# Performance work log

Measured on AMD Instinct MI355X. Metric: run time of the kernel, lower is better.

The kernel has to match this reference:

```python
import jax, jax.numpy as jnp
import numpy as np

B, Q, K, D = 16, 2048, 2048, 512


def setup_inputs() -> dict:
    key = jax.random.key(0)
    kq, kk, kv, kl = jax.random.split(key, 4)
    queries = jax.random.normal(kq, (B, Q, D), dtype=jnp.float32)
    keys = jax.random.normal(kk, (B, K, D), dtype=jnp.float32)
    values = jax.random.normal(kv, (B, K, D), dtype=jnp.float32)
    # lengths in [1, K] so no row is fully masked
    valid_lens = jax.random.randint(kl, (B,), 1, K + 1, dtype=jnp.int32)
    return {"queries": queries, "keys": keys, "values": values, "valid_lens": valid_lens}


def reference(queries, keys, values, valid_lens):
    # scores: [B, Q, K]
    scale = 1.0 / jnp.sqrt(jnp.asarray(queries.shape[-1], queries.dtype))
    scores = jnp.einsum('bqd,bkd->bqk', queries, keys) * scale
    # 1D valid_lens: per-batch key-length mask (positions >= len are masked)
    key_pos = jnp.arange(scores.shape[-1])  # [K]
    mask = key_pos[None, None, :] >= valid_lens[:, None, None]  # [B, 1->Q, K]
    scores = jnp.where(mask, -jnp.inf, scores)
    weights = jax.nn.softmax(scores, axis=-1)  # [B, Q, K]
    # dropout is identity in eval mode (deterministic reference)
    context = jnp.einsum('bqk,bkd->bqd', weights, values)  # [B, Q, D]
    return context, weights
```

## Files before the change

kernel.cpp:

```cpp
#include <hip/hip_runtime.h>
#include <stdint.h>

typedef __bf16 bf16_t;
typedef bf16_t bf16x8 __attribute__((ext_vector_type(8)));
typedef float f32x4 __attribute__((ext_vector_type(4)));

#define NB 16
#define NQ 2048
#define NK 2048
#define ND 512
#define SCALE 0.04419417382415922f

typedef __attribute__((address_space(3))) uint32_t lds_u32;
typedef __attribute__((address_space(1))) const uint32_t glb_u32;

__device__ __forceinline__ float4 ld4(const float* p) { return *(const float4*)p; }

__device__ __forceinline__ f32x4 mfma16(bf16x8 a, bf16x8 b, f32x4 c) {
  return __builtin_amdgcn_mfma_f32_16x16x32_bf16(a, b, c, 0, 0, 0);
}

__global__ __launch_bounds__(256) void qkprep_kernel(const float* __restrict__ Qf,
                                                     const float* __restrict__ Kf,
                                                     bf16_t* __restrict__ Qb,
                                                     bf16_t* __restrict__ Kb) {
  int x = blockIdx.x;
  int b = blockIdx.y;
  const float* src = blockIdx.z ? Kf : Qf;
  bf16_t* dst = blockIdx.z ? Kb : Qb;
  int rt = x >> 4, kt = x & 15;
  const float* s = src + ((size_t)b * 2048 + (size_t)rt * 128) * 512 + kt * 32;
  bf16_t* dtile = dst + (((size_t)b * 16 + rt) * 16 + kt) * 4096;
  int t = threadIdx.x;
#pragma unroll
  for (int i = 0; i < 2; ++i) {
    int d = i * 256 + t;
    int r = d >> 2, slot = d & 3;
    int c = slot ^ ((r >> 1) & 3);
    const float* p = s + (size_t)r * 512 + c * 8;
    float4 v0 = ld4(p), v1 = ld4(p + 4);
    bf16x8 o;
    o[0] = (bf16_t)v0.x; o[1] = (bf16_t)v0.y; o[2] = (bf16_t)v0.z; o[3] = (bf16_t)v0.w;
    o[4] = (bf16_t)v1.x; o[5] = (bf16_t)v1.y; o[6] = (bf16_t)v1.z; o[7] = (bf16_t)v1.w;
    *(bf16x8*)(dtile + (size_t)d * 8) = o;
  }
}

__global__ __launch_bounds__(256) void vt_kernel(const float* __restrict__ V,
                                                 bf16_t* __restrict__ VT,
                                                 const int* __restrict__ lens) {
  int kb = blockIdx.x, b = blockIdx.y;
  if (kb * 32 >= lens[b]) return;
  const float* vsrc = V + ((size_t)b * NK + kb * 32) * ND;
  bf16_t* dst = VT + ((size_t)(b * 64 + kb)) * (512 * 32);
  __shared__ alignas(16) bf16_t Ls[32][128];
  int t = threadIdx.x;
  for (int dbase = 0; dbase < ND; dbase += 128) {
#pragma unroll
    for (int i = 0; i < 4; ++i) {
      int p = i * 256 + t;
      int k = p >> 5, c4 = p & 31;
      float4 v = ld4(vsrc + (size_t)k * ND + dbase + c4 * 4);
      union { bf16_t h[4]; uint2 u; } pk;
      pk.h[0] = (bf16_t)v.x; pk.h[1] = (bf16_t)v.y;
      pk.h[2] = (bf16_t)v.z; pk.h[3] = (bf16_t)v.w;
      *(uint2*)(&Ls[k][c4 * 4]) = pk.u;
    }
    __syncthreads();
    int d = dbase + (t >> 1);
    int h = t & 1;
    int sr = d >> 1;
#pragma unroll
    for (int gg = 0; gg < 2; ++gg) {
      int g = h * 2 + gg;
      bf16x8 v;
#pragma unroll
      for (int j = 0; j < 8; ++j) v[j] = Ls[g * 8 + j][d - dbase];
      int slot = (((d & 1) << 2) | g) ^ (sr & 7);
      *(bf16x8*)(dst + ((size_t)sr * 8 + slot) * 8) = v;
    }
    __syncthreads();
  }
}

__global__ __launch_bounds__(256, 3) void qk_kernel(const bf16_t* __restrict__ Qb,
                                                    const bf16_t* __restrict__ Kb,
                                                    float* __restrict__ P,
                                                    float* __restrict__ psum,
                                                    const int* __restrict__ lens) {
  int bid = blockIdx.x;
  int swz = (bid & 7) * 512 + (bid >> 3);
  int b = swz >> 8;
  int tile = swz & 255;
  int qt = tile >> 4, nt = tile & 15;

  int len = lens[b];
  int q0 = qt * 128;
  int col0 = nt * 128;

  int t = threadIdx.x;
  float* prow = P + ((size_t)b * NQ + q0) * NK;

  if (col0 >= len) {
    float4 z = make_float4(0.f, 0.f, 0.f, 0.f);
#pragma unroll
    for (int i = 0; i < 16; ++i) {
      int p = i * 256 + t;
      int row = p >> 5, c4 = p & 31;
      *(float4*)(prow + (size_t)row * NK + col0 + c4 * 4) = z;
    }
    if (t < 128) psum[((size_t)b * 16 + nt) * NQ + q0 + t] = 0.f;
    return;
  }

  __shared__ alignas(16) bf16_t As[2][4096];
  __shared__ alignas(16) bf16_t Bs[2][4096];
  __shared__ float rsm[128];

  int lane = t & 63;
  int wid = t >> 6;
  int wm = wid >> 1, wn = wid & 1;
  int l15 = lane & 15, l4 = lane >> 4;

  const bf16_t* qtile = Qb + (((size_t)b * 16 + qt) * 16) * 4096;
  const bf16_t* ktile = Kb + (((size_t)b * 16 + nt) * 16) * 4096;

  f32x4 acc[4][4];
  f32x4 zz = {0.f, 0.f, 0.f, 0.f};
#pragma unroll
  for (int mi = 0; mi < 4; ++mi)
#pragma unroll
    for (int ni = 0; ni < 4; ++ni) acc[mi][ni] = zz;

  int eo = wid * 512 + lane * 8;

  auto stage = [&](int kt, int buf) {
    const bf16_t* qa = qtile + (size_t)kt * 4096;
    const bf16_t* ka = ktile + (size_t)kt * 4096;
    bf16_t* la = &As[buf][0];
    bf16_t* lb = &Bs[buf][0];
#pragma unroll
    for (int j = 0; j < 2; ++j) {
      __builtin_amdgcn_global_load_lds((glb_u32*)(qa + j * 2048 + eo),
                                       (lds_u32*)(la + j * 2048 + wid * 512), 16, 0, 0);
      __builtin_amdgcn_global_load_lds((glb_u32*)(ka + j * 2048 + eo),
                                       (lds_u32*)(lb + j * 2048 + wid * 512), 16, 0, 0);
    }
  };

  auto compute = [&](int buf) {
    bf16x8 af[4], bv[4];
#pragma unroll
    for (int mi = 0; mi < 4; ++mi) {
      int row = wm * 64 + mi * 16 + l15;
      int ch = row * 4 + (l4 ^ ((row >> 1) & 3));
      af[mi] = *(const bf16x8*)(&As[buf][ch * 8]);
    }
#pragma unroll
    for (int ni = 0; ni < 4; ++ni) {
      int row = wn * 64 + ni * 16 + l15;
      int ch = row * 4 + (l4 ^ ((row >> 1) & 3));
      bv[ni] = *(const bf16x8*)(&Bs[buf][ch * 8]);
    }
#pragma unroll
    for (int mi = 0; mi < 4; ++mi)
#pragma unroll
      for (int ni = 0; ni < 4; ++ni)
        acc[mi][ni] = mfma16(af[mi], bv[ni], acc[mi][ni]);
  };

  stage(0, 0);
  __syncthreads();
#pragma unroll 1
  for (int kt = 0; kt < 16; ++kt) {
    if (kt + 1 < 16) stage(kt + 1, (kt + 1) & 1);
    compute(kt & 1);
    __syncthreads();
  }

  float rsum[4][4];
#pragma unroll
  for (int mi = 0; mi < 4; ++mi)
#pragma unroll
    for (int r = 0; r < 4; ++r) rsum[mi][r] = 0.f;

#pragma unroll
  for (int mi = 0; mi < 4; ++mi) {
#pragma unroll
    for (int ni = 0; ni < 4; ++ni) {
      int col = col0 + wn * 64 + ni * 16 + l15;
      bool valid = col < len;
#pragma unroll
      for (int r = 0; r < 4; ++r) {
        float e = valid ? __expf(acc[mi][ni][r] * SCALE) : 0.f;
        rsum[mi][r] += e;
        prow[(size_t)(wm * 64 + mi * 16 + l4 * 4 + r) * NK + col] = e;
      }
    }
  }

#pragma unroll
  for (int off = 1; off < 16; off <<= 1)
#pragma unroll
    for (int mi = 0; mi < 4; ++mi)
#pragma unroll
      for (int r = 0; r < 4; ++r)
        rsum[mi][r] += __shfl_xor(rsum[mi][r], off, 64);

  if (wn == 0 && l15 == 0) {
#pragma unroll
    for (int mi = 0; mi < 4; ++mi)
#pragma unroll
      for (int r = 0; r < 4; ++r)
        rsm[wm * 64 + mi * 16 + l4 * 4 + r] = rsum[mi][r];
  }
  __syncthreads();
  if (wn == 1 && l15 == 0) {
#pragma unroll
    for (int mi = 0; mi < 4; ++mi)
#pragma unroll
      for (int r = 0; r < 4; ++r) {
        int row = wm * 64 + mi * 16 + l4 * 4 + r;
        psum[((size_t)b * 16 + nt) * NQ + q0 + row] = rsum[mi][r] + rsm[row];
      }
  }
}

__global__ __launch_bounds__(512, 2) void pv_kernel(float* __restrict__ P,
                                                    const bf16_t* __restrict__ VT,
                                                    float* __restrict__ ctx,
                                                    const float* __restrict__ psum,
                                                    const int* __restrict__ lens) {
  int qt = blockIdx.x, b = blockIdx.y;
  int q0 = qt * 64;
  int len = lens[b];
  int nsteps = (len + 31) >> 5;

  __shared__ alignas(16) bf16_t Ps[2][64 * 32];
  __shared__ alignas(16) bf16_t Vs[2][512 * 32];
  __shared__ float rcp[64];

  int t = threadIdx.x;
  if (t < 64) {
    float s = 0.f;
#pragma unroll
    for (int i = 0; i < 16; ++i) s += psum[((size_t)b * 16 + i) * NQ + q0 + t];
    rcp[t] = 1.0f / s;
  }
  __syncthreads();

  float* prow = P + ((size_t)b * NQ + q0) * NK;
  const bf16_t* vtb = VT + ((size_t)b * 64) * (512 * 32);

  int lane = t & 63, wid = t >> 6;
  int l15 = lane & 15, l4 = lane >> 4;

  f32x4 acc[4][4];
  f32x4 zz = {0.f, 0.f, 0.f, 0.f};
#pragma unroll
  for (int mi = 0; mi < 4; ++mi)
#pragma unroll
    for (int ni = 0; ni < 4; ++ni) acc[mi][ni] = zz;

  int srow = t >> 3, sc4 = t & 7;
  float rr = rcp[srow];

  float4 pld;
  bf16x8 vld[4];

  auto stage_load = [&](int ks) {
    pld = ld4(prow + (size_t)srow * NK + ks * 32 + sc4 * 4);
    const bf16_t* src = vtb + (size_t)ks * (512 * 32);
#pragma unroll
    for (int i = 0; i < 4; ++i)
      vld[i] = *(const bf16x8*)(src + ((size_t)i * 512 + t) * 8);
  };
  auto stage_finish = [&](int ks, int buf) {
    float4 w;
    w.x = pld.x * rr; w.y = pld.y * rr; w.z = pld.z * rr; w.w = pld.w * rr;
    *(float4*)(prow + (size_t)srow * NK + ks * 32 + sc4 * 4) = w;
    int sr = srow >> 1;
    int slot = (((srow & 1) << 2) | (sc4 >> 1)) ^ (sr & 7);
    union { bf16_t h[4]; uint2 u; } pk;
    pk.h[0] = (bf16_t)w.x; pk.h[1] = (bf16_t)w.y;
    pk.h[2] = (bf16_t)w.z; pk.h[3] = (bf16_t)w.w;
    *(uint2*)(&Ps[buf][((size_t)sr * 8 + slot) * 8 + (sc4 & 1) * 4]) = pk.u;
#pragma unroll
    for (int i = 0; i < 4; ++i)
      *(bf16x8*)(&Vs[buf][((size_t)i * 512 + t) * 8]) = vld[i];
  };
  auto compute = [&](int cur) {
    bf16x8 af[4], bv[4];
#pragma unroll
    for (int mi = 0; mi < 4; ++mi) {
      int row = mi * 16 + l15;
      af[mi] = *(const bf16x8*)(&Ps[cur][((row >> 1) * 8 + ((((row & 1) << 2) | l4) ^ ((row >> 1) & 7))) * 8]);
    }
#pragma unroll
    for (int ni = 0; ni < 4; ++ni) {
      int d = wid * 64 + ni * 16 + l15;
      bv[ni] = *(const bf16x8*)(&Vs[cur][((d >> 1) * 8 + ((((d & 1) << 2) | l4) ^ ((d >> 1) & 7))) * 8]);
    }
#pragma unroll
    for (int mi = 0; mi < 4; ++mi)
#pragma unroll
      for (int ni = 0; ni < 4; ++ni)
        acc[mi][ni] = mfma16(af[mi], bv[ni], acc[mi][ni]);
  };

  stage_load(0);
  stage_finish(0, 0);
  __syncthreads();
  for (int ks = 0; ks < nsteps; ++ks) {
    int cur = ks & 1;
    if (ks + 1 < nsteps) stage_load(ks + 1);
    compute(cur);
    if (ks + 1 < nsteps) stage_finish(ks + 1, cur ^ 1);
    __syncthreads();
  }

  float* crow = ctx + ((size_t)b * NQ + q0) * ND + wid * 64;
#pragma unroll
  for (int mi = 0; mi < 4; ++mi)
#pragma unroll
    for (int ni = 0; ni < 4; ++ni)
#pragma unroll
      for (int r = 0; r < 4; ++r)
        crow[(size_t)(mi * 16 + l4 * 4 + r) * ND + ni * 16 + l15] = acc[mi][ni][r];
}

extern "C" void kernel_launch(void* const* d_in, const int* in_sizes, int n_in,
                              void* d_out, int out_size, void* d_ws, size_t ws_size,
                              hipStream_t stream) {
  const float* Q = (const float*)d_in[0];
  const float* K = (const float*)d_in[1];
  const float* V = (const float*)d_in[2];
  const int* lens = (const int*)d_in[3];

  float* ctx = (float*)d_out;
  float* P = ctx + (size_t)NB * NQ * ND;

  float* psum = (float*)d_ws;
  char* base = (char*)d_ws + (size_t)NB * 16 * NQ * sizeof(float);
  bf16_t* Qb = (bf16_t*)base;
  bf16_t* Kb = (bf16_t*)(base + (size_t)NB * NQ * ND * 2);
  bf16_t* VT = (bf16_t*)(base + (size_t)2 * NB * NQ * ND * 2);

  qkprep_kernel<<<dim3(256, 16, 2), 256, 0, stream>>>(Q, K, Qb, Kb);
  vt_kernel<<<dim3(64, 16), 256, 0, stream>>>(V, VT, lens);
  qk_kernel<<<dim3(4096), 256, 0, stream>>>(Qb, Kb, P, psum, lens);
  pv_kernel<<<dim3(32, 16), 512, 0, stream>>>(P, VT, ctx, psum, lens);
}
```

Baseline: 311.4 us.

## Store unnormalized scores as bf16 in upper half of P rows

The QK kernel now writes the exponentiated scores as bf16 into the second half of each fp32 output row instead of full fp32, and skips masked tiles entirely. The PV kernel reads these bf16 values, normalizes them and writes the final fp32 weights, and also zero-fills the masked tail of each row. It sums only the valid partial row sums. This halves intermediate write/read traffic and moves masked zero-fill into PV, at the cost of bf16 rounding in the sums and an in-place aliasing hazard, guarded by an extra barrier on the last steps when the row is full length.

Result: no change. 310.8 us (-0.2%).

```diff
diff --git a/kernel.cpp b/kernel.cpp
--- a/kernel.cpp
+++ b/kernel.cpp
@@ -3,6 +3,7 @@
 
 typedef __bf16 bf16_t;
 typedef bf16_t bf16x8 __attribute__((ext_vector_type(8)));
+typedef bf16_t bf16x4_t __attribute__((ext_vector_type(4)));
 typedef float f32x4 __attribute__((ext_vector_type(4)));
 
 #define NB 16
@@ -97,31 +98,19 @@
   int len = lens[b];
   int q0 = qt * 128;
   int col0 = nt * 128;
-
-  int t = threadIdx.x;
-  float* prow = P + ((size_t)b * NQ + q0) * NK;
-
-  if (col0 >= len) {
-    float4 z = make_float4(0.f, 0.f, 0.f, 0.f);
-#pragma unroll
-    for (int i = 0; i < 16; ++i) {
-      int p = i * 256 + t;
-      int row = p >> 5, c4 = p & 31;
-      *(float4*)(prow + (size_t)row * NK + col0 + c4 * 4) = z;
-    }
-    if (t < 128) psum[((size_t)b * 16 + nt) * NQ + q0 + t] = 0.f;
-    return;
-  }
+  if (col0 >= len) return;
 
   __shared__ alignas(16) bf16_t As[2][4096];
   __shared__ alignas(16) bf16_t Bs[2][4096];
   __shared__ float rsm[128];
 
+  int t = threadIdx.x;
   int lane = t & 63;
   int wid = t >> 6;
   int wm = wid >> 1, wn = wid & 1;
   int l15 = lane & 15, l4 = lane >> 4;
 
+  float* prow = P + ((size_t)b * NQ + q0) * NK;
   const bf16_t* qtile = Qb + (((size_t)b * 16 + qt) * 16) * 4096;
   const bf16_t* ktile = Kb + (((size_t)b * 16 + nt) * 16) * 4096;
 
@@ -193,8 +182,11 @@
 #pragma unroll
       for (int r = 0; r < 4; ++r) {
         float e = valid ? __expf(acc[mi][ni][r] * SCALE) : 0.f;
-        rsum[mi][r] += e;
-        prow[(size_t)(wm * 64 + mi * 16 + l4 * 4 + r) * NK + col] = e;
+        bf16_t eb = (bf16_t)e;
+        rsum[mi][r] += (float)eb;
+        bf16_t* purow =
+            (bf16_t*)(prow + (size_t)(wm * 64 + mi * 16 + l4 * 4 + r) * NK) + 2048;
+        purow[col] = eb;
       }
     }
   }
@@ -235,6 +227,7 @@
   int q0 = qt * 64;
   int len = lens[b];
   int nsteps = (len + 31) >> 5;
+  int nvalid = (len + 127) >> 7;
 
   __shared__ alignas(16) bf16_t Ps[2][64 * 32];
   __shared__ alignas(16) bf16_t Vs[2][512 * 32];
@@ -243,8 +236,7 @@
   int t = threadIdx.x;
   if (t < 64) {
     float s = 0.f;
-#pragma unroll
-    for (int i = 0; i < 16; ++i) s += psum[((size_t)b * 16 + i) * NQ + q0 + t];
+    for (int i = 0; i < nvalid; ++i) s += psum[((size_t)b * 16 + i) * NQ + q0 + t];
     rcp[t] = 1.0f / s;
   }
   __syncthreads();
@@ -264,12 +256,13 @@
 
   int srow = t >> 3, sc4 = t & 7;
   float rr = rcp[srow];
-
-  float4 pld;
+  const bf16_t* purow = (const bf16_t*)(prow + (size_t)srow * NK) + 2048;
+
+  bf16x4_t pld;
   bf16x8 vld[4];
 
   auto stage_load = [&](int ks) {
-    pld = ld4(prow + (size_t)srow * NK + ks * 32 + sc4 * 4);
+    pld = *(const bf16x4_t*)(purow + ks * 32 + sc4 * 4);
     const bf16_t* src = vtb + (size_t)ks * (512 * 32);
 #pragma unroll
     for (int i = 0; i < 4; ++i)
@@ -277,7 +270,8 @@
   };
   auto stage_finish = [&](int ks, int buf) {
     float4 w;
-    w.x = pld.x * rr; w.y = pld.y * rr; w.z = pld.z * rr; w.w = pld.w * rr;
+    w.x = (float)pld[0] * rr; w.y = (float)pld[1] * rr;
+    w.z = (float)pld[2] * rr; w.w = (float)pld[3] * rr;
     *(float4*)(prow + (size_t)srow * NK + ks * 32 + sc4 * 4) = w;
     int sr = srow >> 1;
     int slot = (((srow & 1) << 2) | (sc4 >> 1)) ^ (sr & 7);
@@ -315,8 +309,16 @@
     int cur = ks & 1;
     if (ks + 1 < nsteps) stage_load(ks + 1);
     compute(cur);
+    if (ks == 62 && nsteps == 64) __syncthreads();
     if (ks + 1 < nsteps) stage_finish(ks + 1, cur ^ 1);
     __syncthreads();
+  }
+
+  {
+    float4 z = make_float4(0.f, 0.f, 0.f, 0.f);
+    int tr = t >> 3, tc = t & 7;
+    for (int c = nsteps * 32 + tc * 4; c < NK; c += 32)
+      *(float4*)(prow + (size_t)tr * NK + c) = z;
   }
 
   float* crow = ctx + ((size_t)b * NQ + q0) * ND + wid * 64;
```
